# Optimization experiments

Measured on AMD Instinct MI355X. Metric: run time of the kernel, lower is better.

## Reference

```python
import jax, jax.numpy as jnp
import numpy as np

N, NFEAT, NHID, NCLASS, NHEADS = 3072, 128, 64, 64, 8
ALPHA = 0.2  # LeakyReLU negative slope
NEG = -9e15  # masking value from pyGAT


def gat_layer(h, mask, W, a):
    # h: [N, Fin]; mask: [N, N] bool; W: [H, Fin, Fout]; a: [H, 2*Fout]
    fout = W.shape[-1]
    Wh = jnp.einsum('ni,hio->hno', h, W)            # [H, N, Fout]
    e_src = jnp.einsum('hno,ho->hn', Wh, a[:, :fout])
    e_dst = jnp.einsum('hno,ho->hn', Wh, a[:, fout:])
    e = jax.nn.leaky_relu(e_src[:, :, None] + e_dst[:, None, :], ALPHA)  # [H,N,N]
    e = jnp.where(mask[None], e, NEG)
    att = jax.nn.softmax(e, axis=-1)                 # dropout is identity in eval
    out = jnp.einsum('hnm,hmo->hno', att, Wh)        # [H, N, Fout]
    out = jax.nn.elu(out)                            # concat=True -> elu
    # concat heads along feature dim: [N, H*Fout]
    return out.transpose(1, 0, 2).reshape(h.shape[0], -1)


def setup_inputs() -> dict:
    key = jax.random.key(0)
    ks = jax.random.split(key, 10)
    x = jax.random.normal(ks[0], (N, NFEAT), dtype=jnp.float32)
    adj = (jax.random.uniform(ks[1], (N, N)) < 0.01).astype(jnp.float32)
    adj = jnp.maximum(adj, jnp.eye(N, dtype=jnp.float32))
    hid = NHID * NHEADS
    dims = [(NFEAT, NHID), (hid, NHID), (hid, NHID), (hid, NCLASS)]
    params = {}
    for i, (fin, fout) in enumerate(dims):
        kw, ka = jax.random.split(ks[2 + i])
        params[f'W{i+1}'] = jax.random.normal(kw, (NHEADS, fin, fout), dtype=jnp.float32) * (1.0 / np.sqrt(fin))
        params[f'a{i+1}'] = jax.random.normal(ka, (NHEADS, 2 * fout), dtype=jnp.float32) * 0.1
    return {'x': x, 'adj': adj, **params}


def reference(x, adj, W1, a1, W2, a2, W3, a3, W4, a4):
    mask = adj > 0
    h = gat_layer(x, mask, W1, a1)
    h = gat_layer(h, mask, W2, a2)
    h = gat_layer(h, mask, W3, a3)
    h = gat_layer(h, mask, W4, a4)
    return h  # [N, NHEADS*NCLASS]
```

## Files before the change

kernel.cpp:

```cpp
#include <hip/hip_runtime.h>
#include <math.h>

#define NN 3072
#define NH 8
#define FO 64
#define FCAT 512
#define MAXDEG 128
#define ALPHA 0.2f

typedef __attribute__((ext_vector_type(8))) short bf16x8;
typedef __attribute__((ext_vector_type(4))) float f32x4;

static __device__ __forceinline__ unsigned short f2bf(float v) {
    union { float f; unsigned u; } x; x.f = v;
    unsigned r = x.u + 0x7fffu + ((x.u >> 16) & 1u);
    return (unsigned short)(r >> 16);
}
static __device__ __forceinline__ float bf2f(unsigned short b) {
    union { unsigned u; float f; } x; x.u = ((unsigned)b) << 16;
    return x.f;
}

__global__ __launch_bounds__(256) void prelude_k(const float* __restrict__ x,
                                                 const float* __restrict__ adj,
                                                 const float* __restrict__ W1,
                                                 const float* __restrict__ W2,
                                                 const float* __restrict__ W3,
                                                 const float* __restrict__ W4,
                                                 unsigned short* __restrict__ Ah,
                                                 unsigned short* __restrict__ Al,
                                                 unsigned short* __restrict__ Wth,
                                                 unsigned short* __restrict__ Wtl,
                                                 int* __restrict__ deg,
                                                 int* __restrict__ nbr) {
    __shared__ float t[64][65];
    const int b = blockIdx.x, tid = threadIdx.x;

    if (b < 256) {
        int base = b * 1536 + tid;
        #pragma unroll
        for (int i = 0; i < 6; ++i) {
            int idx = base + i * 256;
            float v = x[idx];
            unsigned short hb = f2bf(v);
            Ah[idx] = hb;
            Al[idx] = f2bf(v - bf2f(hb));
        }
        if (b < 208) {
            const float* W; int K; int local; size_t obase;
            if (b < 16)       { W = W1; K = 128; local = b;       obase = 0; }
            else if (b < 80)  { W = W2; K = 512; local = b - 16;  obase = 65536; }
            else if (b < 144) { W = W3; K = 512; local = b - 80;  obase = 327680; }
            else              { W = W4; K = 512; local = b - 144; obase = 589824; }
            int nkt = K >> 6;
            int h = local / nkt, kt = local - h * nkt;
            int k0 = kt * 64;
            for (int idx = tid; idx < 4096; idx += 256) {
                int r = idx >> 6, c = idx & 63;
                t[r][c] = W[(size_t)h * K * FO + (size_t)(k0 + r) * FO + c];
            }
            __syncthreads();
            for (int idx = tid; idx < 4096; idx += 256) {
                int o = idx >> 6, kk = idx & 63;
                float v = t[kk][o];
                unsigned short hb = f2bf(v);
                size_t dst = obase + (size_t)(h * FO + o) * K + k0 + kk;
                Wth[dst] = hb;
                Wtl[dst] = f2bf(v - bf2f(hb));
            }
        }
    } else {
        int row = (b - 256) * 4 + (tid >> 6);
        int lane = tid & 63;
        const float* arow = adj + (size_t)row * NN;
        int count = 0;
        for (int base = 0; base < NN; base += 64) {
            float v = arow[base + lane];
            unsigned long long m = __ballot(v > 0.0f);
            if (v > 0.0f) {
                int pos = count + __popcll(m & ((1ull << lane) - 1ull));
                if (pos < MAXDEG) nbr[(size_t)row * MAXDEG + pos] = base + lane;
            }
            count += __popcll(m);
        }
        if (lane == 0) deg[row] = count < MAXDEG ? count : MAXDEG;
    }
}

__global__ __launch_bounds__(256, 3) void gemm_ee_k(const unsigned short* __restrict__ Ah,
                                                    const unsigned short* __restrict__ Al,
                                                    const unsigned short* __restrict__ Bh,
                                                    const unsigned short* __restrict__ Bl,
                                                    const float* __restrict__ a,
                                                    float* __restrict__ C,
                                                    float* __restrict__ ee, int K) {
    __shared__ __align__(16) unsigned char smem[30720];
    typedef float CsT[68];
    unsigned short* As_ = (unsigned short*)smem;
    unsigned short* Bs_ = (unsigned short*)(smem + 10240);
    CsT* Cs = reinterpret_cast<CsT*>(smem);

    const int tid = threadIdx.x;
    const int h = blockIdx.x;
    const int r0 = blockIdx.y * 32;
    const int lane = tid & 63;
    const int wid = tid >> 6;
    const int wr = wid >> 1, wc = wid & 1;
    const int lr = lane & 15, lg = lane >> 4;

    const unsigned short* Bhh = Bh + (size_t)h * FO * K;
    const unsigned short* Bll = Bl + (size_t)h * FO * K;

    const int row0 = tid >> 3, cq0 = tid & 7;
    const int off0 = row0 * 80 + ((cq0 ^ (row0 & 7)) * 8);
    const size_t gA0 = (size_t)(r0 + row0) * K + cq0 * 8;
    const size_t gB0 = (size_t)row0 * K + cq0 * 8;
    const size_t gB1 = gB0 + (size_t)32 * K;

    bf16x8 rah, ral, rb0h, rb0l, rb1h, rb1l;

    auto loadg = [&](int k0) {
        rah = *(const bf16x8*)(Ah + gA0 + k0);
        ral = *(const bf16x8*)(Al + gA0 + k0);
        rb0h = *(const bf16x8*)(Bhh + gB0 + k0);
        rb0l = *(const bf16x8*)(Bll + gB0 + k0);
        rb1h = *(const bf16x8*)(Bhh + gB1 + k0);
        rb1l = *(const bf16x8*)(Bll + gB1 + k0);
    };
    auto store_lds = [&]() {
        *(bf16x8*)&As_[off0] = rah;
        *(bf16x8*)&As_[2560 + off0] = ral;
        *(bf16x8*)&Bs_[off0] = rb0h;
        *(bf16x8*)&Bs_[5120 + off0] = rb0l;
        *(bf16x8*)&Bs_[off0 + 2560] = rb1h;
        *(bf16x8*)&Bs_[5120 + off0 + 2560] = rb1l;
    };

    f32x4 acc[2];
    acc[0] = (f32x4){0.f, 0.f, 0.f, 0.f};
    acc[1] = (f32x4){0.f, 0.f, 0.f, 0.f};

    auto mfma_phase = [&]() {
        #pragma unroll
        for (int ks = 0; ks < 2; ++ks) {
            int cq = ks * 4 + lg;
            int arow = wr * 16 + lr;
            int offa = arow * 80 + ((cq ^ (arow & 7)) * 8);
            bf16x8 ah = *(const bf16x8*)&As_[offa];
            bf16x8 al = *(const bf16x8*)&As_[2560 + offa];
            bf16x8 bh[2], bl[2];
            #pragma unroll
            for (int j = 0; j < 2; ++j) {
                int col = wc * 32 + j * 16 + lr;
                int offb = col * 80 + ((cq ^ (col & 7)) * 8);
                bh[j] = *(const bf16x8*)&Bs_[offb];
                bl[j] = *(const bf16x8*)&Bs_[5120 + offb];
            }
            #pragma unroll
            for (int j = 0; j < 2; ++j) {
                acc[j] = __builtin_amdgcn_mfma_f32_16x16x32_bf16(ah, bh[j], acc[j], 0, 0, 0);
                acc[j] = __builtin_amdgcn_mfma_f32_16x16x32_bf16(ah, bl[j], acc[j], 0, 0, 0);
                acc[j] = __builtin_amdgcn_mfma_f32_16x16x32_bf16(al, bh[j], acc[j], 0, 0, 0);
            }
        }
    };

    loadg(0);
    store_lds();
    __syncthreads();
    for (int k0 = 64; k0 < K; k0 += 64) {
        loadg(k0);
        mfma_phase();
        __syncthreads();
        store_lds();
        __syncthreads();
    }
    mfma_phase();
    __syncthreads();

    #pragma unroll
    for (int j = 0; j < 2; ++j)
        #pragma unroll
        for (int r = 0; r < 4; ++r)
            Cs[wr * 16 + lg * 4 + r][wc * 32 + j * 16 + lr] = acc[j][r];
    __syncthreads();

    #pragma unroll
    for (int it = 0; it < 2; ++it) {
        int idx = tid + it * 256;
        int r = idx >> 4, c4 = idx & 15;
        *(float4*)&C[(size_t)(r0 + r) * FCAT + h * FO + c4 * 4] = *(float4*)&Cs[r][c4 * 4];
    }

    {
        int r = tid >> 3, sub = tid & 7;
        const float* av = a + h * 2 * FO;
        float s = 0.0f, dd = 0.0f;
        #pragma unroll
        for (int k = 0; k < 8; ++k) {
            float v = Cs[r][sub * 8 + k];
            s = fmaf(v, av[sub * 8 + k], s);
            dd = fmaf(v, av[FO + sub * 8 + k], dd);
        }
        s += __shfl_xor(s, 1); s += __shfl_xor(s, 2); s += __shfl_xor(s, 4);
        dd += __shfl_xor(dd, 1); dd += __shfl_xor(dd, 2); dd += __shfl_xor(dd, 4);
        if (sub == 0) {
            ee[(size_t)(r0 + r) * 16 + h] = s;
            ee[(size_t)(r0 + r) * 16 + 8 + h] = dd;
        }
    }
}

__global__ __launch_bounds__(256) void attn_agg_k(const float* __restrict__ Wh,
                                                  const float* __restrict__ ee,
                                                  const int* __restrict__ deg,
                                                  const int* __restrict__ nbr,
                                                  float* __restrict__ outp,
                                                  unsigned short* __restrict__ oh,
                                                  unsigned short* __restrict__ ol,
                                                  int write_f32) {
    __shared__ int jbuf[4][MAXDEG];
    __shared__ float pbuf[4][NH][MAXDEG + 4];
    const int ws = threadIdx.x >> 6;
    const int lane = threadIdx.x & 63;
    const int n = blockIdx.x * 4 + ws;
    const int head = lane >> 3;
    const int tt = lane & 7;
    const int d = deg[n];
    const int dpad = (d + 7) & ~7;
    const int* nb = nbr + (size_t)n * MAXDEG;

    for (int t = lane; t < dpad; t += 64) jbuf[ws][t] = (t < d) ? nb[t] : 0;

    const float es_h = ee[(size_t)n * 16 + head];
    float lsum = 0.0f;
    for (int base = 0; base < dpad; base += 8) {
        int t = base + tt;
        int j = jbuf[ws][t];
        float pv = 0.0f;
        if (t < d) {
            float e = es_h + ee[(size_t)j * 16 + 8 + head];
            e = (e > 0.0f) ? e : ALPHA * e;
            pv = __expf(e);
        }
        pbuf[ws][head][t] = pv;
        lsum += pv;
    }
    lsum += __shfl_xor(lsum, 1);
    lsum += __shfl_xor(lsum, 2);
    lsum += __shfl_xor(lsum, 4);

    const int coff = lane * 8;
    float a0 = 0.f, a1 = 0.f, a2 = 0.f, a3 = 0.f;
    float a4 = 0.f, a5 = 0.f, a6 = 0.f, a7 = 0.f;
    for (int t = 0; t < dpad; t += 4) {
        int4 jv = *(const int4*)&jbuf[ws][t];
        float4 pv = *(const float4*)&pbuf[ws][head][t];
        const float* r0 = Wh + (size_t)jv.x * FCAT + coff;
        const float* r1 = Wh + (size_t)jv.y * FCAT + coff;
        const float* r2 = Wh + (size_t)jv.z * FCAT + coff;
        const float* r3 = Wh + (size_t)jv.w * FCAT + coff;
        float4 v00 = *(const float4*)r0, v01 = *(const float4*)(r0 + 4);
        float4 v10 = *(const float4*)r1, v11 = *(const float4*)(r1 + 4);
        float4 v20 = *(const float4*)r2, v21 = *(const float4*)(r2 + 4);
        float4 v30 = *(const float4*)r3, v31 = *(const float4*)(r3 + 4);
        a0 = fmaf(pv.x, v00.x, a0); a1 = fmaf(pv.x, v00.y, a1);
        a2 = fmaf(pv.x, v00.z, a2); a3 = fmaf(pv.x, v00.w, a3);
        a4 = fmaf(pv.x, v01.x, a4); a5 = fmaf(pv.x, v01.y, a5);
        a6 = fmaf(pv.x, v01.z, a6); a7 = fmaf(pv.x, v01.w, a7);
        a0 = fmaf(pv.y, v10.x, a0); a1 = fmaf(pv.y, v10.y, a1);
        a2 = fmaf(pv.y, v10.z, a2); a3 = fmaf(pv.y, v10.w, a3);
        a4 = fmaf(pv.y, v11.x, a4); a5 = fmaf(pv.y, v11.y, a5);
        a6 = fmaf(pv.y, v11.z, a6); a7 = fmaf(pv.y, v11.w, a7);
        a0 = fmaf(pv.z, v20.x, a0); a1 = fmaf(pv.z, v20.y, a1);
        a2 = fmaf(pv.z, v20.z, a2); a3 = fmaf(pv.z, v20.w, a3);
        a4 = fmaf(pv.z, v21.x, a4); a5 = fmaf(pv.z, v21.y, a5);
        a6 = fmaf(pv.z, v21.z, a6); a7 = fmaf(pv.z, v21.w, a7);
        a0 = fmaf(pv.w, v30.x, a0); a1 = fmaf(pv.w, v30.y, a1);
        a2 = fmaf(pv.w, v30.z, a2); a3 = fmaf(pv.w, v30.w, a3);
        a4 = fmaf(pv.w, v31.x, a4); a5 = fmaf(pv.w, v31.y, a5);
        a6 = fmaf(pv.w, v31.z, a6); a7 = fmaf(pv.w, v31.w, a7);
    }

    float inv = 1.0f / lsum;
    float o0 = a0 * inv, o1 = a1 * inv, o2 = a2 * inv, o3 = a3 * inv;
    float o4 = a4 * inv, o5 = a5 * inv, o6 = a6 * inv, o7 = a7 * inv;
    o0 = (o0 > 0.f) ? o0 : (__expf(o0) - 1.f);
    o1 = (o1 > 0.f) ? o1 : (__expf(o1) - 1.f);
    o2 = (o2 > 0.f) ? o2 : (__expf(o2) - 1.f);
    o3 = (o3 > 0.f) ? o3 : (__expf(o3) - 1.f);
    o4 = (o4 > 0.f) ? o4 : (__expf(o4) - 1.f);
    o5 = (o5 > 0.f) ? o5 : (__expf(o5) - 1.f);
    o6 = (o6 > 0.f) ? o6 : (__expf(o6) - 1.f);
    o7 = (o7 > 0.f) ? o7 : (__expf(o7) - 1.f);

    size_t idx = (size_t)n * FCAT + coff;
    if (write_f32) {
        float4 w0 = {o0, o1, o2, o3}, w1 = {o4, o5, o6, o7};
        *(float4*)&outp[idx] = w0;
        *(float4*)&outp[idx + 4] = w1;
    } else {
        unsigned short h0 = f2bf(o0), h1 = f2bf(o1), h2 = f2bf(o2), h3 = f2bf(o3);
        unsigned short h4 = f2bf(o4), h5 = f2bf(o5), h6 = f2bf(o6), h7 = f2bf(o7);
        ushort4 hv0 = {h0, h1, h2, h3}, hv1 = {h4, h5, h6, h7};
        ushort4 lv0 = {f2bf(o0 - bf2f(h0)), f2bf(o1 - bf2f(h1)),
                       f2bf(o2 - bf2f(h2)), f2bf(o3 - bf2f(h3))};
        ushort4 lv1 = {f2bf(o4 - bf2f(h4)), f2bf(o5 - bf2f(h5)),
                       f2bf(o6 - bf2f(h6)), f2bf(o7 - bf2f(h7))};
        *(ushort4*)&oh[idx] = hv0;
        *(ushort4*)&oh[idx + 4] = hv1;
        *(ushort4*)&ol[idx] = lv0;
        *(ushort4*)&ol[idx + 4] = lv1;
    }
}

extern "C" void kernel_launch(void* const* d_in, const int* in_sizes, int n_in,
                              void* d_out, int out_size, void* d_ws, size_t ws_size,
                              hipStream_t stream) {
    const float* x   = (const float*)d_in[0];
    const float* adj = (const float*)d_in[1];
    const float* ap[4] = {(const float*)d_in[3], (const float*)d_in[5],
                          (const float*)d_in[7], (const float*)d_in[9]};
    float* out = (float*)d_out;

    char* p = (char*)d_ws;
    int* deg = (int*)p;              p += (size_t)NN * sizeof(int);
    int* nbr = (int*)p;              p += (size_t)NN * MAXDEG * sizeof(int);
    unsigned short* Ah = (unsigned short*)p; p += (size_t)NN * FCAT * 2;
    unsigned short* Al = (unsigned short*)p; p += (size_t)NN * FCAT * 2;
    float* WhF = (float*)p;          p += (size_t)NN * FCAT * sizeof(float);
    unsigned short* Wth = (unsigned short*)p; p += (size_t)851968 * 2;
    unsigned short* Wtl = (unsigned short*)p; p += (size_t)851968 * 2;
    float* ee = (float*)p;           p += (size_t)NN * 16 * sizeof(float);

    prelude_k<<<1024, 256, 0, stream>>>(x, adj,
                                        (const float*)d_in[2], (const float*)d_in[4],
                                        (const float*)d_in[6], (const float*)d_in[8],
                                        Ah, Al, Wth, Wtl, deg, nbr);

    const size_t woff[4] = {0, 65536, 327680, 589824};
    int K = 128;
    for (int L = 0; L < 4; ++L) {
        dim3 g(NH, NN / 32);
        gemm_ee_k<<<g, 256, 0, stream>>>(Ah, Al, Wth + woff[L], Wtl + woff[L],
                                         ap[L], WhF, ee, K);
        attn_agg_k<<<NN / 4, 256, 0, stream>>>(WhF, ee, deg, nbr,
                                               out, Ah, Al, L == 3 ? 1 : 0);
        K = FCAT;
    }
}
```

Before: 131.8 us.

## Split each node's neighbor aggregation across two wavefronts with LDS reduction

```diff
diff --git a/kernel.cpp b/kernel.cpp
--- a/kernel.cpp
+++ b/kernel.cpp
@@ -219,43 +219,52 @@
                                                   unsigned short* __restrict__ oh,
                                                   unsigned short* __restrict__ ol,
                                                   int write_f32) {
-    __shared__ int jbuf[4][MAXDEG];
-    __shared__ float pbuf[4][NH][MAXDEG + 4];
+    __shared__ int jbuf[2][MAXDEG + 16];
+    __shared__ float pbuf[2][NH][MAXDEG + 20];
+    __shared__ float lsums[2][2][NH];
+    __shared__ float accbuf[2][512];
     const int ws = threadIdx.x >> 6;
     const int lane = threadIdx.x & 63;
-    const int n = blockIdx.x * 4 + ws;
+    const int nbi = ws >> 1;
+    const int p = ws & 1;
+    const int n = blockIdx.x * 2 + nbi;
     const int head = lane >> 3;
     const int tt = lane & 7;
     const int d = deg[n];
-    const int dpad = (d + 7) & ~7;
+    const int dpad = (d + 15) & ~15;
+    const int half = dpad >> 1;
+    const int t0 = p * half, t1 = t0 + half;
     const int* nb = nbr + (size_t)n * MAXDEG;
 
-    for (int t = lane; t < dpad; t += 64) jbuf[ws][t] = (t < d) ? nb[t] : 0;
+    for (int t = t0 + lane; t < t1; t += 64) jbuf[nbi][t] = (t < d) ? nb[t] : 0;
 
     const float es_h = ee[(size_t)n * 16 + head];
     float lsum = 0.0f;
-    for (int base = 0; base < dpad; base += 8) {
+    for (int base = t0; base < t1; base += 8) {
         int t = base + tt;
-        int j = jbuf[ws][t];
+        int j = jbuf[nbi][t];
         float pv = 0.0f;
         if (t < d) {
             float e = es_h + ee[(size_t)j * 16 + 8 + head];
             e = (e > 0.0f) ? e : ALPHA * e;
             pv = __expf(e);
         }
-        pbuf[ws][head][t] = pv;
+        pbuf[nbi][head][t] = pv;
         lsum += pv;
     }
     lsum += __shfl_xor(lsum, 1);
     lsum += __shfl_xor(lsum, 2);
     lsum += __shfl_xor(lsum, 4);
+    if (tt == 0) lsums[nbi][p][head] = lsum;
+    __syncthreads();
+    const float lsum_tot = lsums[nbi][0][head] + lsums[nbi][1][head];
 
     const int coff = lane * 8;
     float a0 = 0.f, a1 = 0.f, a2 = 0.f, a3 = 0.f;
     float a4 = 0.f, a5 = 0.f, a6 = 0.f, a7 = 0.f;
-    for (int t = 0; t < dpad; t += 4) {
-        int4 jv = *(const int4*)&jbuf[ws][t];
-        float4 pv = *(const float4*)&pbuf[ws][head][t];
+    for (int t = t0; t < t1; t += 4) {
+        int4 jv = *(const int4*)&jbuf[nbi][t];
+        float4 pv = *(const float4*)&pbuf[nbi][head][t];
         const float* r0 = Wh + (size_t)jv.x * FCAT + coff;
         const float* r1 = Wh + (size_t)jv.y * FCAT + coff;
         const float* r2 = Wh + (size_t)jv.z * FCAT + coff;
@@ -282,35 +291,47 @@
         a6 = fmaf(pv.w, v31.z, a6); a7 = fmaf(pv.w, v31.w, a7);
     }
 
-    float inv = 1.0f / lsum;
-    float o0 = a0 * inv, o1 = a1 * inv, o2 = a2 * inv, o3 = a3 * inv;
-    float o4 = a4 * inv, o5 = a5 * inv, o6 = a6 * inv, o7 = a7 * inv;
-    o0 = (o0 > 0.f) ? o0 : (__expf(o0) - 1.f);
-    o1 = (o1 > 0.f) ? o1 : (__expf(o1) - 1.f);
-    o2 = (o2 > 0.f) ? o2 : (__expf(o2) - 1.f);
-    o3 = (o3 > 0.f) ? o3 : (__expf(o3) - 1.f);
-    o4 = (o4 > 0.f) ? o4 : (__expf(o4) - 1.f);
-    o5 = (o5 > 0.f) ? o5 : (__expf(o5) - 1.f);
-    o6 = (o6 > 0.f) ? o6 : (__expf(o6) - 1.f);
-    o7 = (o7 > 0.f) ? o7 : (__expf(o7) - 1.f);
-
-    size_t idx = (size_t)n * FCAT + coff;
-    if (write_f32) {
-        float4 w0 = {o0, o1, o2, o3}, w1 = {o4, o5, o6, o7};
-        *(float4*)&outp[idx] = w0;
-        *(float4*)&outp[idx + 4] = w1;
-    } else {
-        unsigned short h0 = f2bf(o0), h1 = f2bf(o1), h2 = f2bf(o2), h3 = f2bf(o3);
-        unsigned short h4 = f2bf(o4), h5 = f2bf(o5), h6 = f2bf(o6), h7 = f2bf(o7);
-        ushort4 hv0 = {h0, h1, h2, h3}, hv1 = {h4, h5, h6, h7};
-        ushort4 lv0 = {f2bf(o0 - bf2f(h0)), f2bf(o1 - bf2f(h1)),
-                       f2bf(o2 - bf2f(h2)), f2bf(o3 - bf2f(h3))};
-        ushort4 lv1 = {f2bf(o4 - bf2f(h4)), f2bf(o5 - bf2f(h5)),
-                       f2bf(o6 - bf2f(h6)), f2bf(o7 - bf2f(h7))};
-        *(ushort4*)&oh[idx] = hv0;
-        *(ushort4*)&oh[idx + 4] = hv1;
-        *(ushort4*)&ol[idx] = lv0;
-        *(ushort4*)&ol[idx + 4] = lv1;
+    if (p == 1) {
+        float* ab = &accbuf[nbi][coff];
+        ab[0] = a0; ab[1] = a1; ab[2] = a2; ab[3] = a3;
+        ab[4] = a4; ab[5] = a5; ab[6] = a6; ab[7] = a7;
+    }
+    __syncthreads();
+    if (p == 0) {
+        const float* ab = &accbuf[nbi][coff];
+        a0 += ab[0]; a1 += ab[1]; a2 += ab[2]; a3 += ab[3];
+        a4 += ab[4]; a5 += ab[5]; a6 += ab[6]; a7 += ab[7];
+
+        float inv = 1.0f / lsum_tot;
+        float o0 = a0 * inv, o1 = a1 * inv, o2 = a2 * inv, o3 = a3 * inv;
+        float o4 = a4 * inv, o5 = a5 * inv, o6 = a6 * inv, o7 = a7 * inv;
+        o0 = (o0 > 0.f) ? o0 : (__expf(o0) - 1.f);
+        o1 = (o1 > 0.f) ? o1 : (__expf(o1) - 1.f);
+        o2 = (o2 > 0.f) ? o2 : (__expf(o2) - 1.f);
+        o3 = (o3 > 0.f) ? o3 : (__expf(o3) - 1.f);
+        o4 = (o4 > 0.f) ? o4 : (__expf(o4) - 1.f);
+        o5 = (o5 > 0.f) ? o5 : (__expf(o5) - 1.f);
+        o6 = (o6 > 0.f) ? o6 : (__expf(o6) - 1.f);
+        o7 = (o7 > 0.f) ? o7 : (__expf(o7) - 1.f);
+
+        size_t idx = (size_t)n * FCAT + coff;
+        if (write_f32) {
+            float4 w0 = {o0, o1, o2, o3}, w1 = {o4, o5, o6, o7};
+            *(float4*)&outp[idx] = w0;
+            *(float4*)&outp[idx + 4] = w1;
+        } else {
+            unsigned short h0 = f2bf(o0), h1 = f2bf(o1), h2 = f2bf(o2), h3 = f2bf(o3);
+            unsigned short h4 = f2bf(o4), h5 = f2bf(o5), h6 = f2bf(o6), h7 = f2bf(o7);
+            ushort4 hv0 = {h0, h1, h2, h3}, hv1 = {h4, h5, h6, h7};
+            ushort4 lv0 = {f2bf(o0 - bf2f(h0)), f2bf(o1 - bf2f(h1)),
+                           f2bf(o2 - bf2f(h2)), f2bf(o3 - bf2f(h3))};
+            ushort4 lv1 = {f2bf(o4 - bf2f(h4)), f2bf(o5 - bf2f(h5)),
+                           f2bf(o6 - bf2f(h6)), f2bf(o7 - bf2f(h7))};
+            *(ushort4*)&oh[idx] = hv0;
+            *(ushort4*)&oh[idx + 4] = hv1;
+            *(ushort4*)&ol[idx] = lv0;
+            *(ushort4*)&ol[idx + 4] = lv1;
+        }
     }
 }
 
@@ -344,7 +365,7 @@
         dim3 g(NH, NN / 32);
         gemm_ee_k<<<g, 256, 0, stream>>>(Ah, Al, Wth + woff[L], Wtl + woff[L],
                                          ap[L], WhF, ee, K);
-        attn_agg_k<<<NN / 4, 256, 0, stream>>>(WhF, ee, deg, nbr,
+        attn_agg_k<<<NN / 2, 256, 0, stream>>>(WhF, ee, deg, nbr,
                                                out, Ah, Al, L == 3 ? 1 : 0);
         K = FCAT;
     }
```

Result: slower. 138.7 us (+5.2%).
